# Optimization experiments

Hardware: AMD Instinct MI355X
Metric: run time of the kernel (lower is better)

Reference implementation:

```python
import jax, jax.numpy as jnp
import numpy as np

B, S, D, H = 2, 2048, 1024, 16
DK = D // H


def setup_inputs() -> dict:
    key = jax.random.key(0)
    ks = jax.random.split(key, 11)
    scale = 1.0 / np.sqrt(D)
    inp = {
        'q': jax.random.normal(ks[0], (B, S, D), jnp.float32),
        'k': jax.random.normal(ks[1], (B, S, D), jnp.float32),
        'v': jax.random.normal(ks[2], (B, S, D), jnp.float32),
        'mask': jnp.tril(jnp.ones((S, S), jnp.int32))[None, None],  # [1,1,S,S] causal
        'w_q': jax.random.normal(ks[3], (D, D), jnp.float32) * scale,
        'b_q': jax.random.normal(ks[4], (D,), jnp.float32) * scale,
        'w_k': jax.random.normal(ks[5], (D, D), jnp.float32) * scale,
        'b_k': jax.random.normal(ks[6], (D,), jnp.float32) * scale,
        'w_v': jax.random.normal(ks[7], (D, D), jnp.float32) * scale,
        'b_v': jax.random.normal(ks[8], (D,), jnp.float32) * scale,
        'w_o': jax.random.normal(ks[9], (D, D), jnp.float32) * scale,
        'b_o': jax.random.normal(ks[10], (D,), jnp.float32) * scale,
    }
    return inp


def reference(q, k, v, mask, w_q, b_q, w_k, b_k, w_v, b_v, w_o, b_o):
    # Linear projections (torch Linear: x @ W^T + b; here weights stored as [D_in, D_out])
    query = q @ w_q + b_q  # [B,S,D]
    key_ = k @ w_k + b_k
    value = v @ w_v + b_v
    # split heads -> [B,H,S,DK]
    def split(x):
        return x.reshape(B, S, H, DK).transpose(0, 2, 1, 3)
    qh, kh, vh = split(query), split(key_), split(value)
    scores = jnp.einsum('bhqd,bhkd->bhqk', qh, kh) / jnp.sqrt(jnp.float32(DK))
    scores = jnp.where(mask == 0, jnp.float32(-1e9), scores)
    attn = jax.nn.softmax(scores, axis=-1)  # dropout p=0.0 -> identity
    out = jnp.einsum('bhqk,bhkd->bhqd', attn, vh)  # [B,H,S,DK]
    out = out.transpose(0, 2, 1, 3).reshape(B, S, D)
    return out @ w_o + b_o
```

## Files before the change

### kernel.cpp

```cpp
#include <hip/hip_runtime.h>

typedef unsigned short u16;
typedef unsigned int u32;
typedef __attribute__((ext_vector_type(8))) short short8;
typedef __attribute__((ext_vector_type(4))) float f32x4;
typedef __attribute__((ext_vector_type(16))) float f32x16;
typedef __attribute__((ext_vector_type(4))) float float4v;
typedef __attribute__((ext_vector_type(4))) u16 u16x4;
typedef __attribute__((ext_vector_type(2))) u32 u32x2;

#define DEV static __device__ __forceinline__

static constexpr int S_LEN = 2048;
static constexpr int D_MODEL = 1024;
static constexpr int N_HEADS = 16;
static constexpr int DK = 64;
static constexpr float LOG2E = 1.4426950408889634f;
static constexpr float SM_SHIFT = 12.0f;

#if defined(__has_builtin)
#if __has_builtin(__builtin_amdgcn_exp2f)
#define EXP2(x) __builtin_amdgcn_exp2f(x)
#else
#define EXP2(x) exp2f(x)
#endif
#else
#define EXP2(x) exp2f(x)
#endif

DEV u16 f2bf(float f) {
  u32 u = __builtin_bit_cast(u32, f);
  u32 r = (u + 0x7FFFu + ((u >> 16) & 1u)) >> 16;
  return (u16)r;
}

DEV u32 pk2bf(float lo, float hi) {
  u32 d;
  asm("v_cvt_pk_bf16_f32 %0, %1, %2" : "=v"(d) : "v"(lo), "v"(hi));
  return d;
}

DEV void swap32(u32& a, u32& b) {
  asm volatile("v_permlane32_swap_b32 %0, %1" : "+v"(a), "+v"(b));
}

DEV short8 mk8(u32 w0, u32 w1, u32 w2, u32 w3) {
  union { u32 u[4]; short8 s; } t;
  t.u[0] = w0; t.u[1] = w1; t.u[2] = w2; t.u[3] = w3;
  return t.s;
}

DEV void async16(const void* g, void* l) {
  __builtin_amdgcn_global_load_lds(
      (const __attribute__((address_space(1))) u32*)g,
      (__attribute__((address_space(3))) u32*)l, 16, 0, 0);
}

DEV short8 lds_frag(const u16* tile, int row, int byteInRow) {
  const char* p = (const char*)tile + row * 128 + (byteInRow ^ ((row & 7) << 4));
  return *(const short8*)p;
}

DEV f32x4 mfma16(short8 a, short8 b, f32x4 c) {
  return __builtin_amdgcn_mfma_f32_16x16x32_bf16(a, b, c, 0, 0, 0);
}

DEV f32x16 mfma32(short8 a, short8 b, f32x16 c) {
  return __builtin_amdgcn_mfma_f32_32x32x16_bf16(a, b, c, 0, 0, 0);
}

__global__ void k_prep(const float* __restrict__ q, const float* __restrict__ k,
                       const float* __restrict__ v,
                       const float* __restrict__ wq, const float* __restrict__ wk,
                       const float* __restrict__ wv, const float* __restrict__ wo,
                       u16* __restrict__ xq, u16* __restrict__ xk, u16* __restrict__ xv,
                       u16* __restrict__ tq, u16* __restrict__ tk,
                       u16* __restrict__ tv, u16* __restrict__ to_) {
  __shared__ u16 t[64][65];
  const int z = blockIdx.y;
  if (z < 3) {
    const float* src = z == 0 ? q : (z == 1 ? k : v);
    u16* dst = z == 0 ? xq : (z == 1 ? xk : xv);
    int i = (blockIdx.x * 256 + threadIdx.x) * 4;
    const int stride = 512 * 256 * 4;
    for (; i < 4096 * 1024; i += stride) {
      float4v f = *(const float4v*)(src + i);
      u16x4 o;
      o[0] = f2bf(f[0]); o[1] = f2bf(f[1]); o[2] = f2bf(f[2]); o[3] = f2bf(f[3]);
      *(u16x4*)(dst + i) = o;
    }
  } else {
    if (blockIdx.x >= 256) return;
    const int zz = z - 3;
    const float* W = zz == 0 ? wq : (zz == 1 ? wk : (zz == 2 ? wv : wo));
    u16* Wt = zz == 0 ? tq : (zz == 1 ? tk : (zz == 2 ? tv : to_));
    const int n0 = (blockIdx.x & 15) * 64;
    const int k0 = (blockIdx.x >> 4) * 64;
    const int tid = threadIdx.x;
    const int c = tid & 63, r0 = tid >> 6;
#pragma unroll
    for (int j = 0; j < 16; ++j) {
      int r = r0 + j * 4;
      t[r][c] = f2bf(W[(size_t)(k0 + r) * D_MODEL + n0 + c]);
    }
    __syncthreads();
#pragma unroll
    for (int j = 0; j < 16; ++j) {
      int r = r0 + j * 4;
      Wt[(size_t)(n0 + r) * D_MODEL + k0 + c] = t[c][r];
    }
  }
}

__global__ __launch_bounds__(256, 3) void k_gemm3(
    const u16* __restrict__ Xq, const u16* __restrict__ Xk, const u16* __restrict__ Xv,
    const u16* __restrict__ Wtq, const u16* __restrict__ Wtk, const u16* __restrict__ Wtv,
    const float* __restrict__ bq, const float* __restrict__ bk, const float* __restrict__ bv,
    u16* __restrict__ Qh, u16* __restrict__ Kh, u16* __restrict__ Vtp) {
  const int lin = blockIdx.x + (blockIdx.y << 5) + (blockIdx.z << 8);
  const int wg = (lin & 7) * 96 + (lin >> 3);
  const int bx = wg & 31, by = (wg >> 5) & 7;
  const int z = wg >> 8;
  const u16* A = z == 0 ? Xq : (z == 1 ? Xk : Xv);
  const u16* Bt = z == 0 ? Wtq : (z == 1 ? Wtk : Wtv);
  const float* bias = z == 0 ? bq : (z == 1 ? bk : bv);
  u16* obf = z == 0 ? Qh : (z == 1 ? Kh : Vtp);
  const float scale = z == 0 ? 0.125f * LOG2E : 1.0f;

  __shared__ __align__(16) u16 As[128 * 64];
  __shared__ __align__(16) u16 Bs[128 * 64];
  const int tid = threadIdx.x;
  const int lane = tid & 63, w = tid >> 6;
  const int l15 = lane & 15, l4 = lane >> 4;
  const int bm = bx * 128, bn = by * 128;
  const int wr = (w >> 1) * 64, wc = (w & 1) * 64;
  const int sr = tid >> 3, sc8 = tid & 7;
  f32x4 acc[4][4] = {};

  for (int k0 = 0; k0 < 1024; k0 += 64) {
    __syncthreads();
#pragma unroll
    for (int j = 0; j < 4; ++j) {
      int row = sr + j * 32;
      int col = (sc8 ^ (row & 7)) << 3;
      async16(A + (size_t)(bm + row) * 1024 + k0 + col, (char*)As + tid * 16 + j * 4096);
      async16(Bt + (size_t)(bn + row) * 1024 + k0 + col, (char*)Bs + tid * 16 + j * 4096);
    }
    __syncthreads();
    short8 af[4][2], bfv[4][2];
#pragma unroll
    for (int mi = 0; mi < 4; ++mi)
#pragma unroll
      for (int kk = 0; kk < 2; ++kk)
        af[mi][kk] = lds_frag(As, wr + mi * 16 + l15, kk * 64 + l4 * 16);
#pragma unroll
    for (int ni = 0; ni < 4; ++ni)
#pragma unroll
      for (int kk = 0; kk < 2; ++kk)
        bfv[ni][kk] = lds_frag(Bs, wc + ni * 16 + l15, kk * 64 + l4 * 16);
#pragma unroll
    for (int kk = 0; kk < 2; ++kk)
#pragma unroll
      for (int mi = 0; mi < 4; ++mi)
#pragma unroll
        for (int ni = 0; ni < 4; ++ni)
          acc[mi][ni] = mfma16(af[mi][kk], bfv[ni][kk], acc[mi][ni]);
  }

#pragma unroll
  for (int mi = 0; mi < 4; ++mi)
#pragma unroll
    for (int ni = 0; ni < 4; ++ni) {
      const int row0 = bm + wr + mi * 16 + l4 * 4;
      const int col = bn + wc + ni * 16 + l15;
      const int h = col >> 6, dk = col & 63;
      const int b = row0 >> 11, s0 = row0 & 2047;
      if (z == 2) {
        u16x4 pk;
#pragma unroll
        for (int r = 0; r < 4; ++r) pk[r] = f2bf(acc[mi][ni][r] + bias[col]);
        *(u16x4*)(obf + ((size_t)((b * N_HEADS + h) * DK + dk)) * S_LEN + s0) = pk;
      } else {
#pragma unroll
        for (int r = 0; r < 4; ++r) {
          float vv = (acc[mi][ni][r] + bias[col]) * scale;
          obf[(((size_t)(b * N_HEADS + h) * S_LEN + s0 + r) << 6) + dk] = f2bf(vv);
        }
      }
    }
}

__global__ __launch_bounds__(256, 3) void k_gemmO(
    const u16* __restrict__ A, const u16* __restrict__ Bt,
    const float* __restrict__ bias, float* __restrict__ ofp) {
  const int lin = blockIdx.x + (blockIdx.y << 5);
  const int wg = (lin & 7) * 64 + (lin >> 3);
  const int bx = wg & 31, by = wg >> 5;
  __shared__ __align__(16) u16 As[128 * 64];
  __shared__ __align__(16) u16 Bs[64 * 64];
  const int tid = threadIdx.x;
  const int lane = tid & 63, w = tid >> 6;
  const int l15 = lane & 15, l4 = lane >> 4;
  const int bm = bx * 128, bn = by * 64;
  const int wr = w * 32;
  const int sr = tid >> 3, sc8 = tid & 7;
  f32x4 acc[2][4] = {};

  for (int k0 = 0; k0 < 1024; k0 += 64) {
    __syncthreads();
#pragma unroll
    for (int j = 0; j < 4; ++j) {
      int row = sr + j * 32;
      int col = (sc8 ^ (row & 7)) << 3;
      async16(A + (size_t)(bm + row) * 1024 + k0 + col, (char*)As + tid * 16 + j * 4096);
      if (j < 2)
        async16(Bt + (size_t)(bn + row) * 1024 + k0 + col, (char*)Bs + tid * 16 + j * 4096);
    }
    __syncthreads();
    short8 af[2][2], bfv[4][2];
#pragma unroll
    for (int mi = 0; mi < 2; ++mi)
#pragma unroll
      for (int kk = 0; kk < 2; ++kk)
        af[mi][kk] = lds_frag(As, wr + mi * 16 + l15, kk * 64 + l4 * 16);
#pragma unroll
    for (int ni = 0; ni < 4; ++ni)
#pragma unroll
      for (int kk = 0; kk < 2; ++kk)
        bfv[ni][kk] = lds_frag(Bs, ni * 16 + l15, kk * 64 + l4 * 16);
#pragma unroll
    for (int kk = 0; kk < 2; ++kk)
#pragma unroll
      for (int mi = 0; mi < 2; ++mi)
#pragma unroll
        for (int ni = 0; ni < 4; ++ni)
          acc[mi][ni] = mfma16(af[mi][kk], bfv[ni][kk], acc[mi][ni]);
  }

#pragma unroll
  for (int mi = 0; mi < 2; ++mi)
#pragma unroll
    for (int ni = 0; ni < 4; ++ni)
#pragma unroll
      for (int r = 0; r < 4; ++r) {
        int row = bm + wr + mi * 16 + l4 * 4 + r;
        int col = bn + ni * 16 + l15;
        ofp[(size_t)row * D_MODEL + col] = acc[mi][ni][r] + bias[col];
      }
}

__global__ __launch_bounds__(128, 4) void k_attn(
    const u16* __restrict__ Qh, const u16* __restrict__ Kh,
    const u16* __restrict__ Vt, u16* __restrict__ Om) {
  __shared__ __align__(16) u16 Ks[2][64 * 64];
  __shared__ __align__(16) u16 Vs[2][64 * 64];
  const int tid = threadIdx.x;
  const int lane = tid & 63, w = tid >> 6;
  const int l31 = lane & 31, hf = (lane >> 5) & 1;
  const int bh = blockIdx.x;
  const int y = blockIdx.y, y0 = y & 7, qd = y >> 3;
  const int jq = qd == 0 ? y0 : (qd == 1 ? 31 - y0 : (qd == 2 ? 8 + y0 : 23 - y0));
  const int q0 = jq * 64;
  const int qw = q0 + w * 32;
  const u16* Qb = Qh + (size_t)bh * S_LEN * DK;
  const u16* Kb = Kh + (size_t)bh * S_LEN * DK;
  const u16* Vb = Vt + (size_t)bh * DK * S_LEN;
  const int sc8 = tid & 7;

  auto stage = [&](int t0, int buf) {
#pragma unroll
    for (int j = 0; j < 4; ++j) {
      int row = (tid >> 3) + j * 16;
      int col = (sc8 ^ (row & 7)) << 3;
      async16(Kb + (size_t)(t0 + row) * DK + col, (char*)Ks[buf] + tid * 16 + j * 2048);
      async16(Vb + (size_t)row * S_LEN + t0 + col, (char*)Vs[buf] + tid * 16 + j * 2048);
    }
  };

  short8 qB[4];
#pragma unroll
  for (int cc = 0; cc < 4; ++cc)
    qB[cc] = *(const short8*)(Qb + (size_t)(qw + l31) * DK + cc * 16 + hf * 8);

  f32x16 od0 = {}, od1 = {};
  float rs = 0.f;
  const int nt = jq + 1;

  stage(0, 0);
  __syncthreads();
  int cur = 0;
#pragma unroll 1
  for (int ti = 0; ti < nt; ++ti) {
    const int t0 = ti << 6;
    if (ti + 1 < nt) stage(t0 + 64, cur ^ 1);

#pragma unroll
    for (int kt = 0; kt < 2; ++kt) {
      f32x16 s;
#pragma unroll
      for (int r = 0; r < 16; ++r) s[r] = -SM_SHIFT;
      __builtin_amdgcn_s_setprio(1);
#pragma unroll
      for (int cc = 0; cc < 4; ++cc) {
        short8 kf = lds_frag(Ks[cur], kt * 32 + l31, cc * 32 + hf * 16);
        s = mfma32(kf, qB[cc], s);
      }
      __builtin_amdgcn_s_setprio(0);

      if (t0 + kt * 32 + 31 > qw) {
        const int qrow = qw + l31;
#pragma unroll
        for (int r = 0; r < 16; ++r) {
          int kr = t0 + kt * 32 + ((r & 3) + 8 * (r >> 2) + 4 * hf);
          if (kr > qrow) s[r] = -1e30f;
        }
      }

#pragma unroll
      for (int r = 0; r < 16; ++r) s[r] = EXP2(s[r]);
      {
        float t01 = (s[0] + s[1]) + (s[2] + s[3]);
        float t23 = (s[4] + s[5]) + (s[6] + s[7]);
        float t45 = (s[8] + s[9]) + (s[10] + s[11]);
        float t67 = (s[12] + s[13]) + (s[14] + s[15]);
        rs += (t01 + t23) + (t45 + t67);
      }

      u32 a0 = pk2bf(s[0], s[1]), b0 = pk2bf(s[4], s[5]);
      u32 c0 = pk2bf(s[2], s[3]), d0 = pk2bf(s[6], s[7]);
      swap32(a0, b0); swap32(c0, d0);
      short8 pbA = mk8(a0, c0, b0, d0);
      u32 e0 = pk2bf(s[8], s[9]), f0 = pk2bf(s[12], s[13]);
      u32 g0 = pk2bf(s[10], s[11]), h0 = pk2bf(s[14], s[15]);
      swap32(e0, f0); swap32(g0, h0);
      short8 pbB = mk8(e0, g0, f0, h0);

      __builtin_amdgcn_s_setprio(1);
      {
        short8 v00 = lds_frag(Vs[cur], l31, kt * 64 + hf * 16);
        short8 v10 = lds_frag(Vs[cur], 32 + l31, kt * 64 + hf * 16);
        od0 = mfma32(v00, pbA, od0);
        od1 = mfma32(v10, pbA, od1);
        short8 v01 = lds_frag(Vs[cur], l31, kt * 64 + 32 + hf * 16);
        short8 v11 = lds_frag(Vs[cur], 32 + l31, kt * 64 + 32 + hf * 16);
        od0 = mfma32(v01, pbB, od0);
        od1 = mfma32(v11, pbB, od1);
      }
      __builtin_amdgcn_s_setprio(0);
    }
    __syncthreads();
    cur ^= 1;
  }

  rs += __shfl_xor(rs, 32);

  const float inv = 1.f / rs;
  const int b = bh >> 4, hd = bh & 15;
  u16* dst = Om + (size_t)(b * S_LEN + qw + l31) * D_MODEL + hd * DK;
#pragma unroll
  for (int rr = 0; rr < 4; ++rr) {
    u16x4 o0, o1;
#pragma unroll
    for (int i = 0; i < 4; ++i) {
      o0[i] = f2bf(od0[rr * 4 + i] * inv);
      o1[i] = f2bf(od1[rr * 4 + i] * inv);
    }
    *(u16x4*)(dst + rr * 8 + 4 * hf) = o0;
    *(u16x4*)(dst + 32 + rr * 8 + 4 * hf) = o1;
  }
}

extern "C" void kernel_launch(void* const* d_in, const int* in_sizes, int n_in,
                              void* d_out, int out_size, void* d_ws, size_t ws_size,
                              hipStream_t stream) {
  (void)in_sizes; (void)n_in; (void)out_size; (void)ws_size;
  const float* q  = (const float*)d_in[0];
  const float* k  = (const float*)d_in[1];
  const float* v  = (const float*)d_in[2];
  const float* wq = (const float*)d_in[4];
  const float* bq = (const float*)d_in[5];
  const float* wk = (const float*)d_in[6];
  const float* bk = (const float*)d_in[7];
  const float* wv = (const float*)d_in[8];
  const float* bv = (const float*)d_in[9];
  const float* wo = (const float*)d_in[10];
  const float* bo = (const float*)d_in[11];
  float* out = (float*)d_out;

  char* ws = (char*)d_ws;
  const size_t XB = (size_t)4096 * 1024 * 2;
  const size_t WB = (size_t)1024 * 1024 * 2;
  u16* Xq  = (u16*)(ws);
  u16* Xk  = (u16*)(ws + XB);
  u16* Xv  = (u16*)(ws + 2 * XB);
  u16* Wtq = (u16*)(ws + 3 * XB);
  u16* Wtk = (u16*)(ws + 3 * XB + WB);
  u16* Wtv = (u16*)(ws + 3 * XB + 2 * WB);
  u16* Wto = (u16*)(ws + 3 * XB + 3 * WB);
  u16* Qh  = (u16*)(ws + 3 * XB + 4 * WB);
  u16* Kh  = (u16*)(ws + 4 * XB + 4 * WB);
  u16* Vtp = (u16*)(ws + 5 * XB + 4 * WB);
  u16* Om  = Xq;

  k_prep<<<dim3(512, 7), 256, 0, stream>>>(q, k, v, wq, wk, wv, wo,
                                           Xq, Xk, Xv, Wtq, Wtk, Wtv, Wto);
  k_gemm3<<<dim3(32, 8, 3), 256, 0, stream>>>(Xq, Xk, Xv, Wtq, Wtk, Wtv,
                                              bq, bk, bv, Qh, Kh, Vtp);
  k_attn<<<dim3(32, 32), 128, 0, stream>>>(Qh, Kh, Vtp, Om);
  k_gemmO<<<dim3(32, 16), 256, 0, stream>>>(Om, Wto, bo, out);
}
```

Before: 120.0 us.

## Pair causal query tiles per block and split long tile's keys across wave teams

Each attention block now handles two query tiles, y and 31-y, with 4 waves in two teams, sharing the K/V staging. While both tiles are active, each team processes its own tile over full key blocks. Once the short tile finishes, team 0 writes it out and joins the long tile, with each team taking one 32-key half per block, and partial outputs are reduced through LDS at the end. The intent is to balance causal work per block and halve the global K/V loads shared by the paired tiles, at the cost of an extra reduction and more registers and threads per block.

After: 150.9 us. +25.8%, slower.

```diff
diff --git a/kernel.cpp b/kernel.cpp
--- a/kernel.cpp
+++ b/kernel.cpp
@@ -7,7 +7,6 @@
 typedef __attribute__((ext_vector_type(16))) float f32x16;
 typedef __attribute__((ext_vector_type(4))) float float4v;
 typedef __attribute__((ext_vector_type(4))) u16 u16x4;
-typedef __attribute__((ext_vector_type(2))) u32 u32x2;
 
 #define DEV static __device__ __forceinline__
 
@@ -249,7 +248,7 @@
       }
 }
 
-__global__ __launch_bounds__(128, 4) void k_attn(
+__global__ __launch_bounds__(256, 4) void k_attn(
     const u16* __restrict__ Qh, const u16* __restrict__ Kh,
     const u16* __restrict__ Vt, u16* __restrict__ Om) {
   __shared__ __align__(16) u16 Ks[2][64 * 64];
@@ -257,96 +256,124 @@
   const int tid = threadIdx.x;
   const int lane = tid & 63, w = tid >> 6;
   const int l31 = lane & 31, hf = (lane >> 5) & 1;
+  const int team = w >> 1, tw = w & 1;
   const int bh = blockIdx.x;
-  const int y = blockIdx.y, y0 = y & 7, qd = y >> 3;
-  const int jq = qd == 0 ? y0 : (qd == 1 ? 31 - y0 : (qd == 2 ? 8 + y0 : 23 - y0));
-  const int q0 = jq * 64;
-  const int qw = q0 + w * 32;
+  const int y = blockIdx.y;
+  const int jqA = y, jqB = 31 - y;
+  const int ntA = jqA + 1, ntB = jqB + 1;
   const u16* Qb = Qh + (size_t)bh * S_LEN * DK;
   const u16* Kb = Kh + (size_t)bh * S_LEN * DK;
   const u16* Vb = Vt + (size_t)bh * DK * S_LEN;
   const int sc8 = tid & 7;
+  const int b = bh >> 4, hd = bh & 15;
 
   auto stage = [&](int t0, int buf) {
 #pragma unroll
-    for (int j = 0; j < 4; ++j) {
-      int row = (tid >> 3) + j * 16;
+    for (int j = 0; j < 2; ++j) {
+      int row = (tid >> 3) + j * 32;
       int col = (sc8 ^ (row & 7)) << 3;
-      async16(Kb + (size_t)(t0 + row) * DK + col, (char*)Ks[buf] + tid * 16 + j * 2048);
-      async16(Vb + (size_t)row * S_LEN + t0 + col, (char*)Vs[buf] + tid * 16 + j * 2048);
+      async16(Kb + (size_t)(t0 + row) * DK + col, (char*)Ks[buf] + tid * 16 + j * 4096);
+      async16(Vb + (size_t)row * S_LEN + t0 + col, (char*)Vs[buf] + tid * 16 + j * 4096);
     }
   };
 
+  int qw = (team ? jqB : jqA) * 64 + tw * 32;
   short8 qB[4];
 #pragma unroll
   for (int cc = 0; cc < 4; ++cc)
     qB[cc] = *(const short8*)(Qb + (size_t)(qw + l31) * DK + cc * 16 + hf * 8);
 
-  f32x16 od0 = {}, od1 = {};
+  f32x16 od0, od1;
+#pragma unroll
+  for (int r = 0; r < 16; ++r) { od0[r] = 0.f; od1[r] = 0.f; }
   float rs = 0.f;
-  const int nt = jq + 1;
+  int cur = 0;
+
+  auto half = [&](int kt, int t0) {
+    f32x16 s;
+#pragma unroll
+    for (int r = 0; r < 16; ++r) s[r] = -SM_SHIFT;
+    __builtin_amdgcn_s_setprio(1);
+#pragma unroll
+    for (int cc = 0; cc < 4; ++cc) {
+      short8 kf = lds_frag(Ks[cur], kt * 32 + l31, cc * 32 + hf * 16);
+      s = mfma32(kf, qB[cc], s);
+    }
+    __builtin_amdgcn_s_setprio(0);
+    if (t0 + kt * 32 + 31 > qw) {
+      const int qrow = qw + l31;
+#pragma unroll
+      for (int r = 0; r < 16; ++r) {
+        int kr = t0 + kt * 32 + ((r & 3) + 8 * (r >> 2) + 4 * hf);
+        if (kr > qrow) s[r] = -1e30f;
+      }
+    }
+#pragma unroll
+    for (int r = 0; r < 16; ++r) s[r] = EXP2(s[r]);
+    {
+      float t01 = (s[0] + s[1]) + (s[2] + s[3]);
+      float t23 = (s[4] + s[5]) + (s[6] + s[7]);
+      float t45 = (s[8] + s[9]) + (s[10] + s[11]);
+      float t67 = (s[12] + s[13]) + (s[14] + s[15]);
+      rs += (t01 + t23) + (t45 + t67);
+    }
+    u32 a0 = pk2bf(s[0], s[1]), b0 = pk2bf(s[4], s[5]);
+    u32 c0 = pk2bf(s[2], s[3]), d0 = pk2bf(s[6], s[7]);
+    swap32(a0, b0); swap32(c0, d0);
+    short8 pbA = mk8(a0, c0, b0, d0);
+    u32 e0 = pk2bf(s[8], s[9]), f0 = pk2bf(s[12], s[13]);
+    u32 g0 = pk2bf(s[10], s[11]), h0 = pk2bf(s[14], s[15]);
+    swap32(e0, f0); swap32(g0, h0);
+    short8 pbB = mk8(e0, g0, f0, h0);
+    __builtin_amdgcn_s_setprio(1);
+    {
+      short8 v00 = lds_frag(Vs[cur], l31, kt * 64 + hf * 16);
+      short8 v10 = lds_frag(Vs[cur], 32 + l31, kt * 64 + hf * 16);
+      od0 = mfma32(v00, pbA, od0);
+      od1 = mfma32(v10, pbA, od1);
+      short8 v01 = lds_frag(Vs[cur], l31, kt * 64 + 32 + hf * 16);
+      short8 v11 = lds_frag(Vs[cur], 32 + l31, kt * 64 + 32 + hf * 16);
+      od0 = mfma32(v01, pbB, od0);
+      od1 = mfma32(v11, pbB, od1);
+    }
+    __builtin_amdgcn_s_setprio(0);
+  };
 
   stage(0, 0);
   __syncthreads();
-  int cur = 0;
 #pragma unroll 1
-  for (int ti = 0; ti < nt; ++ti) {
+  for (int ti = 0; ti < ntB; ++ti) {
     const int t0 = ti << 6;
-    if (ti + 1 < nt) stage(t0 + 64, cur ^ 1);
-
-#pragma unroll
-    for (int kt = 0; kt < 2; ++kt) {
-      f32x16 s;
-#pragma unroll
-      for (int r = 0; r < 16; ++r) s[r] = -SM_SHIFT;
-      __builtin_amdgcn_s_setprio(1);
-#pragma unroll
-      for (int cc = 0; cc < 4; ++cc) {
-        short8 kf = lds_frag(Ks[cur], kt * 32 + l31, cc * 32 + hf * 16);
-        s = mfma32(kf, qB[cc], s);
-      }
-      __builtin_amdgcn_s_setprio(0);
-
-      if (t0 + kt * 32 + 31 > qw) {
-        const int qrow = qw + l31;
-#pragma unroll
-        for (int r = 0; r < 16; ++r) {
-          int kr = t0 + kt * 32 + ((r & 3) + 8 * (r >> 2) + 4 * hf);
-          if (kr > qrow) s[r] = -1e30f;
+    if (ti + 1 < ntB) stage(t0 + 64, cur ^ 1);
+
+    if (ti < ntA) {
+      half(0, t0);
+      half(1, t0);
+    } else {
+      if (team == 0 && ti == ntA) {
+        float rsf = rs + __shfl_xor(rs, 32);
+        float inv = 1.f / rsf;
+        u16* dst = Om + (size_t)(b * S_LEN + qw + l31) * D_MODEL + hd * DK;
+#pragma unroll
+        for (int rr = 0; rr < 4; ++rr) {
+          u16x4 o0, o1;
+#pragma unroll
+          for (int i = 0; i < 4; ++i) {
+            o0[i] = f2bf(od0[rr * 4 + i] * inv);
+            o1[i] = f2bf(od1[rr * 4 + i] * inv);
+          }
+          *(u16x4*)(dst + rr * 8 + 4 * hf) = o0;
+          *(u16x4*)(dst + 32 + rr * 8 + 4 * hf) = o1;
         }
-      }
-
-#pragma unroll
-      for (int r = 0; r < 16; ++r) s[r] = EXP2(s[r]);
-      {
-        float t01 = (s[0] + s[1]) + (s[2] + s[3]);
-        float t23 = (s[4] + s[5]) + (s[6] + s[7]);
-        float t45 = (s[8] + s[9]) + (s[10] + s[11]);
-        float t67 = (s[12] + s[13]) + (s[14] + s[15]);
-        rs += (t01 + t23) + (t45 + t67);
-      }
-
-      u32 a0 = pk2bf(s[0], s[1]), b0 = pk2bf(s[4], s[5]);
-      u32 c0 = pk2bf(s[2], s[3]), d0 = pk2bf(s[6], s[7]);
-      swap32(a0, b0); swap32(c0, d0);
-      short8 pbA = mk8(a0, c0, b0, d0);
-      u32 e0 = pk2bf(s[8], s[9]), f0 = pk2bf(s[12], s[13]);
-      u32 g0 = pk2bf(s[10], s[11]), h0 = pk2bf(s[14], s[15]);
-      swap32(e0, f0); swap32(g0, h0);
-      short8 pbB = mk8(e0, g0, f0, h0);
-
-      __builtin_amdgcn_s_setprio(1);
-      {
-        short8 v00 = lds_frag(Vs[cur], l31, kt * 64 + hf * 16);
-        short8 v10 = lds_frag(Vs[cur], 32 + l31, kt * 64 + hf * 16);
-        od0 = mfma32(v00, pbA, od0);
-        od1 = mfma32(v10, pbA, od1);
-        short8 v01 = lds_frag(Vs[cur], l31, kt * 64 + 32 + hf * 16);
-        short8 v11 = lds_frag(Vs[cur], 32 + l31, kt * 64 + 32 + hf * 16);
-        od0 = mfma32(v01, pbB, od0);
-        od1 = mfma32(v11, pbB, od1);
-      }
-      __builtin_amdgcn_s_setprio(0);
+#pragma unroll
+        for (int r = 0; r < 16; ++r) { od0[r] = 0.f; od1[r] = 0.f; }
+        rs = 0.f;
+        qw = jqB * 64 + tw * 32;
+#pragma unroll
+        for (int cc = 0; cc < 4; ++cc)
+          qB[cc] = *(const short8*)(Qb + (size_t)(qw + l31) * DK + cc * 16 + hf * 8);
+      }
+      half(team, t0);
     }
     __syncthreads();
     cur ^= 1;
@@ -354,19 +381,46 @@
 
   rs += __shfl_xor(rs, 32);
 
-  const float inv = 1.f / rs;
-  const int b = bh >> 4, hd = bh & 15;
-  u16* dst = Om + (size_t)(b * S_LEN + qw + l31) * D_MODEL + hd * DK;
-#pragma unroll
-  for (int rr = 0; rr < 4; ++rr) {
-    u16x4 o0, o1;
-#pragma unroll
-    for (int i = 0; i < 4; ++i) {
-      o0[i] = f2bf(od0[rr * 4 + i] * inv);
-      o1[i] = f2bf(od1[rr * 4 + i] * inv);
-    }
-    *(u16x4*)(dst + rr * 8 + 4 * hf) = o0;
-    *(u16x4*)(dst + 32 + rr * 8 + 4 * hf) = o1;
+  float* cb = (float*)Ks;
+  float* cr = (float*)Vs;
+  if (team == 0) {
+    float4v* dv = (float4v*)cb + ((w * 64 + lane) * 8);
+#pragma unroll
+    for (int rr = 0; rr < 4; ++rr) {
+      float4v v0, v1;
+#pragma unroll
+      for (int i = 0; i < 4; ++i) { v0[i] = od0[rr * 4 + i]; v1[i] = od1[rr * 4 + i]; }
+      dv[rr] = v0;
+      dv[4 + rr] = v1;
+    }
+    cr[w * 64 + lane] = rs;
+  }
+  __syncthreads();
+  if (team == 1) {
+    const float4v* dv = (const float4v*)cb + (((w - 2) * 64 + lane) * 8);
+#pragma unroll
+    for (int rr = 0; rr < 4; ++rr) {
+      float4v v0 = dv[rr], v1 = dv[4 + rr];
+#pragma unroll
+      for (int i = 0; i < 4; ++i) {
+        od0[rr * 4 + i] += v0[i];
+        od1[rr * 4 + i] += v1[i];
+      }
+    }
+    rs += cr[(w - 2) * 64 + lane];
+    const float inv = 1.f / rs;
+    u16* dst = Om + (size_t)(b * S_LEN + qw + l31) * D_MODEL + hd * DK;
+#pragma unroll
+    for (int rr = 0; rr < 4; ++rr) {
+      u16x4 o0, o1;
+#pragma unroll
+      for (int i = 0; i < 4; ++i) {
+        o0[i] = f2bf(od0[rr * 4 + i] * inv);
+        o1[i] = f2bf(od1[rr * 4 + i] * inv);
+      }
+      *(u16x4*)(dst + rr * 8 + 4 * hf) = o0;
+      *(u16x4*)(dst + 32 + rr * 8 + 4 * hf) = o1;
+    }
   }
 }
 
@@ -406,6 +460,6 @@
                                            Xq, Xk, Xv, Wtq, Wtk, Wtv, Wto);
   k_gemm3<<<dim3(32, 8, 3), 256, 0, stream>>>(Xq, Xk, Xv, Wtq, Wtk, Wtv,
                                               bq, bk, bv, Qh, Kh, Vtp);
-  k_attn<<<dim3(32, 32), 128, 0, stream>>>(Qh, Kh, Vtp, Om);
+  k_attn<<<dim3(32, 16), 256, 0, stream>>>(Qh, Kh, Vtp, Om);
   k_gemmO<<<dim3(32, 16), 256, 0, stream>>>(Om, Wto, bo, out);
 }
```

## Split attention KV tile across four waves with LDS reduction of partial outputs

Applied to the files above, without the earlier changes.

The attention block grows from 2 to 4 waves. Each pair of waves now splits the 64-key tile into two 32-key halves instead of one wave looping over both halves. Partial output accumulators and row sums are combined through LDS after the loop, and one wave writes the result. The aim is more parallelism per block and better latency hiding, at the cost of a final LDS reduction, an extra barrier, and more threads contending for the same tiles.

New measurement: 104.9 us, median of 3. 1.14x faster.

```diff
diff --git a/kernel.cpp b/kernel.cpp
--- a/kernel.cpp
+++ b/kernel.cpp
@@ -7,7 +7,6 @@
 typedef __attribute__((ext_vector_type(16))) float f32x16;
 typedef __attribute__((ext_vector_type(4))) float float4v;
 typedef __attribute__((ext_vector_type(4))) u16 u16x4;
-typedef __attribute__((ext_vector_type(2))) u32 u32x2;
 
 #define DEV static __device__ __forceinline__
 
@@ -249,7 +248,7 @@
       }
 }
 
-__global__ __launch_bounds__(128, 4) void k_attn(
+__global__ __launch_bounds__(256, 4) void k_attn(
     const u16* __restrict__ Qh, const u16* __restrict__ Kh,
     const u16* __restrict__ Vt, u16* __restrict__ Om) {
   __shared__ __align__(16) u16 Ks[2][64 * 64];
@@ -257,23 +256,25 @@
   const int tid = threadIdx.x;
   const int lane = tid & 63, w = tid >> 6;
   const int l31 = lane & 31, hf = (lane >> 5) & 1;
+  const int qh = w & 1, kvh = w >> 1;
   const int bh = blockIdx.x;
   const int y = blockIdx.y, y0 = y & 7, qd = y >> 3;
   const int jq = qd == 0 ? y0 : (qd == 1 ? 31 - y0 : (qd == 2 ? 8 + y0 : 23 - y0));
   const int q0 = jq * 64;
-  const int qw = q0 + w * 32;
+  const int qw = q0 + qh * 32;
   const u16* Qb = Qh + (size_t)bh * S_LEN * DK;
   const u16* Kb = Kh + (size_t)bh * S_LEN * DK;
   const u16* Vb = Vt + (size_t)bh * DK * S_LEN;
   const int sc8 = tid & 7;
+  const int b = bh >> 4, hd = bh & 15;
 
   auto stage = [&](int t0, int buf) {
 #pragma unroll
-    for (int j = 0; j < 4; ++j) {
-      int row = (tid >> 3) + j * 16;
+    for (int j = 0; j < 2; ++j) {
+      int row = (tid >> 3) + j * 32;
       int col = (sc8 ^ (row & 7)) << 3;
-      async16(Kb + (size_t)(t0 + row) * DK + col, (char*)Ks[buf] + tid * 16 + j * 2048);
-      async16(Vb + (size_t)row * S_LEN + t0 + col, (char*)Vs[buf] + tid * 16 + j * 2048);
+      async16(Kb + (size_t)(t0 + row) * DK + col, (char*)Ks[buf] + tid * 16 + j * 4096);
+      async16(Vb + (size_t)row * S_LEN + t0 + col, (char*)Vs[buf] + tid * 16 + j * 4096);
     }
   };
 
@@ -282,7 +283,9 @@
   for (int cc = 0; cc < 4; ++cc)
     qB[cc] = *(const short8*)(Qb + (size_t)(qw + l31) * DK + cc * 16 + hf * 8);
 
-  f32x16 od0 = {}, od1 = {};
+  f32x16 od0, od1;
+#pragma unroll
+  for (int r = 0; r < 16; ++r) { od0[r] = 0.f; od1[r] = 0.f; }
   float rs = 0.f;
   const int nt = jq + 1;
 
@@ -294,79 +297,103 @@
     const int t0 = ti << 6;
     if (ti + 1 < nt) stage(t0 + 64, cur ^ 1);
 
-#pragma unroll
-    for (int kt = 0; kt < 2; ++kt) {
-      f32x16 s;
-#pragma unroll
-      for (int r = 0; r < 16; ++r) s[r] = -SM_SHIFT;
-      __builtin_amdgcn_s_setprio(1);
-#pragma unroll
-      for (int cc = 0; cc < 4; ++cc) {
-        short8 kf = lds_frag(Ks[cur], kt * 32 + l31, cc * 32 + hf * 16);
-        s = mfma32(kf, qB[cc], s);
+    f32x16 s;
+#pragma unroll
+    for (int r = 0; r < 16; ++r) s[r] = -SM_SHIFT;
+    __builtin_amdgcn_s_setprio(1);
+#pragma unroll
+    for (int cc = 0; cc < 4; ++cc) {
+      short8 kf = lds_frag(Ks[cur], kvh * 32 + l31, cc * 32 + hf * 16);
+      s = mfma32(kf, qB[cc], s);
+    }
+    __builtin_amdgcn_s_setprio(0);
+
+    if (t0 + kvh * 32 + 31 > qw) {
+      const int qrow = qw + l31;
+#pragma unroll
+      for (int r = 0; r < 16; ++r) {
+        int kr = t0 + kvh * 32 + ((r & 3) + 8 * (r >> 2) + 4 * hf);
+        if (kr > qrow) s[r] = -1e30f;
       }
-      __builtin_amdgcn_s_setprio(0);
-
-      if (t0 + kt * 32 + 31 > qw) {
-        const int qrow = qw + l31;
-#pragma unroll
-        for (int r = 0; r < 16; ++r) {
-          int kr = t0 + kt * 32 + ((r & 3) + 8 * (r >> 2) + 4 * hf);
-          if (kr > qrow) s[r] = -1e30f;
-        }
+    }
+
+#pragma unroll
+    for (int r = 0; r < 16; ++r) s[r] = EXP2(s[r]);
+    {
+      float t01 = (s[0] + s[1]) + (s[2] + s[3]);
+      float t23 = (s[4] + s[5]) + (s[6] + s[7]);
+      float t45 = (s[8] + s[9]) + (s[10] + s[11]);
+      float t67 = (s[12] + s[13]) + (s[14] + s[15]);
+      rs += (t01 + t23) + (t45 + t67);
+    }
+
+    u32 a0 = pk2bf(s[0], s[1]), b0 = pk2bf(s[4], s[5]);
+    u32 c0 = pk2bf(s[2], s[3]), d0 = pk2bf(s[6], s[7]);
+    swap32(a0, b0); swap32(c0, d0);
+    short8 pbA = mk8(a0, c0, b0, d0);
+    u32 e0 = pk2bf(s[8], s[9]), f0 = pk2bf(s[12], s[13]);
+    u32 g0 = pk2bf(s[10], s[11]), h0 = pk2bf(s[14], s[15]);
+    swap32(e0, f0); swap32(g0, h0);
+    short8 pbB = mk8(e0, g0, f0, h0);
+
+    __builtin_amdgcn_s_setprio(1);
+    {
+      short8 v00 = lds_frag(Vs[cur], l31, kvh * 64 + hf * 16);
+      short8 v10 = lds_frag(Vs[cur], 32 + l31, kvh * 64 + hf * 16);
+      od0 = mfma32(v00, pbA, od0);
+      od1 = mfma32(v10, pbA, od1);
+      short8 v01 = lds_frag(Vs[cur], l31, kvh * 64 + 32 + hf * 16);
+      short8 v11 = lds_frag(Vs[cur], 32 + l31, kvh * 64 + 32 + hf * 16);
+      od0 = mfma32(v01, pbB, od0);
+      od1 = mfma32(v11, pbB, od1);
+    }
+    __builtin_amdgcn_s_setprio(0);
+    __syncthreads();
+    cur ^= 1;
+  }
+
+  rs += __shfl_xor(rs, 32);
+
+  float* cb = (float*)Ks;
+  float* cr = (float*)Vs;
+  if (kvh == 0) {
+    float4v* dv = (float4v*)cb + ((qh * 64 + lane) * 8);
+#pragma unroll
+    for (int rr = 0; rr < 4; ++rr) {
+      float4v v0, v1;
+#pragma unroll
+      for (int i = 0; i < 4; ++i) { v0[i] = od0[rr * 4 + i]; v1[i] = od1[rr * 4 + i]; }
+      dv[rr] = v0;
+      dv[4 + rr] = v1;
+    }
+    cr[qh * 64 + lane] = rs;
+  }
+  __syncthreads();
+  if (kvh == 1) {
+    const float4v* dv = (const float4v*)cb + ((qh * 64 + lane) * 8);
+#pragma unroll
+    for (int rr = 0; rr < 4; ++rr) {
+      float4v v0 = dv[rr], v1 = dv[4 + rr];
+#pragma unroll
+      for (int i = 0; i < 4; ++i) {
+        od0[rr * 4 + i] += v0[i];
+        od1[rr * 4 + i] += v1[i];
       }
-
-#pragma unroll
-      for (int r = 0; r < 16; ++r) s[r] = EXP2(s[r]);
-      {
-        float t01 = (s[0] + s[1]) + (s[2] + s[3]);
-        float t23 = (s[4] + s[5]) + (s[6] + s[7]);
-        float t45 = (s[8] + s[9]) + (s[10] + s[11]);
-        float t67 = (s[12] + s[13]) + (s[14] + s[15]);
-        rs += (t01 + t23) + (t45 + t67);
+    }
+    rs += cr[qh * 64 + lane];
+    const float inv = 1.f / rs;
+    u16* dst = Om + (size_t)(b * S_LEN + qw + l31) * D_MODEL + hd * DK;
+#pragma unroll
+    for (int rr = 0; rr < 4; ++rr) {
+      u16x4 o0, o1;
+#pragma unroll
+      for (int i = 0; i < 4; ++i) {
+        o0[i] = f2bf(od0[rr * 4 + i] * inv);
+        o1[i] = f2bf(od1[rr * 4 + i] * inv);
       }
-
-      u32 a0 = pk2bf(s[0], s[1]), b0 = pk2bf(s[4], s[5]);
-      u32 c0 = pk2bf(s[2], s[3]), d0 = pk2bf(s[6], s[7]);
-      swap32(a0, b0); swap32(c0, d0);
-      short8 pbA = mk8(a0, c0, b0, d0);
-      u32 e0 = pk2bf(s[8], s[9]), f0 = pk2bf(s[12], s[13]);
-      u32 g0 = pk2bf(s[10], s[11]), h0 = pk2bf(s[14], s[15]);
-      swap32(e0, f0); swap32(g0, h0);
-      short8 pbB = mk8(e0, g0, f0, h0);
-
-      __builtin_amdgcn_s_setprio(1);
-      {
-        short8 v00 = lds_frag(Vs[cur], l31, kt * 64 + hf * 16);
-        short8 v10 = lds_frag(Vs[cur], 32 + l31, kt * 64 + hf * 16);
-        od0 = mfma32(v00, pbA, od0);
-        od1 = mfma32(v10, pbA, od1);
-        short8 v01 = lds_frag(Vs[cur], l31, kt * 64 + 32 + hf * 16);
-        short8 v11 = lds_frag(Vs[cur], 32 + l31, kt * 64 + 32 + hf * 16);
-        od0 = mfma32(v01, pbB, od0);
-        od1 = mfma32(v11, pbB, od1);
-      }
-      __builtin_amdgcn_s_setprio(0);
-    }
-    __syncthreads();
-    cur ^= 1;
-  }
-
-  rs += __shfl_xor(rs, 32);
-
-  const float inv = 1.f / rs;
-  const int b = bh >> 4, hd = bh & 15;
-  u16* dst = Om + (size_t)(b * S_LEN + qw + l31) * D_MODEL + hd * DK;
-#pragma unroll
-  for (int rr = 0; rr < 4; ++rr) {
-    u16x4 o0, o1;
-#pragma unroll
-    for (int i = 0; i < 4; ++i) {
-      o0[i] = f2bf(od0[rr * 4 + i] * inv);
-      o1[i] = f2bf(od1[rr * 4 + i] * inv);
-    }
-    *(u16x4*)(dst + rr * 8 + 4 * hf) = o0;
-    *(u16x4*)(dst + 32 + rr * 8 + 4 * hf) = o1;
+      *(u16x4*)(dst + rr * 8 + 4 * hf) = o0;
+      *(u16x4*)(dst + 32 + rr * 8 + 4 * hf) = o1;
+    }
   }
 }
 
@@ -406,6 +433,6 @@
                                            Xq, Xk, Xv, Wtq, Wtk, Wtv, Wto);
   k_gemm3<<<dim3(32, 8, 3), 256, 0, stream>>>(Xq, Xk, Xv, Wtq, Wtk, Wtv,
                                               bq, bk, bv, Qh, Kh, Vtp);
-  k_attn<<<dim3(32, 32), 128, 0, stream>>>(Qh, Kh, Vtp, Om);
+  k_attn<<<dim3(32, 32), 256, 0, stream>>>(Qh, Kh, Vtp, Om);
   k_gemmO<<<dim3(32, 16), 256, 0, stream>>>(Om, Wto, bo, out);
 }
```
